# Kernel optimization log

Hardware: AMD Instinct MI355X
Metric: run time of the kernel (lower is better)

Reference implementation:

```python
import jax, jax.numpy as jnp
import numpy as np

B, F, N = 32, 10, 512   # batch_num, win_size (all_feature), node_num
E = 8192                # edges per graph
INTER = 256             # GAT inter_dim
HEADS = 2
NEG_SLOPE = 0.2
BN_EPS = 1e-5


def setup_inputs() -> dict:
    key = jax.random.key(0)
    ks = jax.random.split(key, 16)
    data = jax.random.normal(ks[0], (B, F, N), dtype=jnp.float32)
    # loop-free random edges: src != dst (matches PyG remove_self_loops + add_self_loops)
    dst = jax.random.randint(ks[1], (E,), 0, N)
    off = jax.random.randint(ks[2], (E,), 1, N)
    src = (dst + off) % N
    org_edge_index = jnp.stack([src, dst]).astype(jnp.int64)
    g = 0.05
    return {
        "data": data,
        "org_edge_index": org_edge_index,
        "W1": jax.random.normal(ks[3], (F, HEADS * INTER), dtype=jnp.float32) * g,
        "as1": jax.random.normal(ks[4], (HEADS, INTER), dtype=jnp.float32) * g,
        "ad1": jax.random.normal(ks[5], (HEADS, INTER), dtype=jnp.float32) * g,
        "b1": jnp.zeros((HEADS * INTER,), dtype=jnp.float32),
        "W2": jax.random.normal(ks[6], (HEADS * INTER, HEADS * INTER), dtype=jnp.float32) * g,
        "as2": jax.random.normal(ks[7], (HEADS, INTER), dtype=jnp.float32) * g,
        "ad2": jax.random.normal(ks[8], (HEADS, INTER), dtype=jnp.float32) * g,
        "b2": jnp.zeros((HEADS * INTER,), dtype=jnp.float32),
        "Wfc": jax.random.normal(ks[9], (HEADS * INTER, 1), dtype=jnp.float32) * g,
        "bfc": jnp.zeros((1,), dtype=jnp.float32),
        "gamma": jnp.ones((1,), dtype=jnp.float32),
        "beta": jnp.zeros((1,), dtype=jnp.float32),
    }


def _gat_conv(x, src, dst, W, a_src, a_dst, b):
    # PyG GATConv (v1), concat=True, negative_slope=0.2
    n = x.shape[0]
    H, C = a_src.shape
    h = (x @ W).reshape(n, H, C)                       # [n, H, C]
    al_s = jnp.einsum('nhc,hc->nh', h, a_src)          # [n, H]
    al_d = jnp.einsum('nhc,hc->nh', h, a_dst)
    e = jax.nn.leaky_relu(al_s[src] + al_d[dst], NEG_SLOPE)  # [Etot, H]
    emax = jax.ops.segment_max(e, dst, num_segments=n)       # segment softmax over dst
    ex = jnp.exp(e - emax[dst])
    denom = jax.ops.segment_sum(ex, dst, num_segments=n)
    alpha = ex / (denom[dst] + 1e-16)                  # [Etot, H]
    msg = h[src] * alpha[:, :, None]                   # [Etot, H, C]
    out = jax.ops.segment_sum(msg, dst, num_segments=n)
    return out.reshape(n, H * C) + b


def reference(data, org_edge_index, W1, as1, ad1, b1, W2, as2, ad2, b2,
              Wfc, bfc, gamma, beta):
    b_num, feat, n_num = data.shape
    x = data.reshape(-1, feat)                         # faithful to x.view(-1, all_feature)
    total = b_num * n_num
    # batched edge index: repeat with per-batch node offsets
    offs = jnp.arange(b_num, dtype=org_edge_index.dtype) * n_num
    be = (org_edge_index[:, None, :] + offs[None, :, None]).reshape(2, -1)
    loops = jnp.arange(total, dtype=org_edge_index.dtype)  # add_self_loops
    src = jnp.concatenate([be[0], loops])
    dst = jnp.concatenate([be[1], loops])
    x1 = _gat_conv(x, src, dst, W1, as1, ad1, b1)      # dropout = identity (eval)
    x2 = _gat_conv(x1, src, dst, W2, as2, ad2, b2)
    y = x2 @ Wfc + bfc                                 # [total, 1]
    # BatchNorm1d(1), eval mode: running_mean=0, running_var=1
    y = y * (gamma / jnp.sqrt(1.0 + BN_EPS)) + beta
    y = jax.nn.relu(y)
    return y.reshape(-1, 1, n_num)                     # [B, 1, N]
```

## Files before the change

### kernel.cpp

```cpp
#include <hip/hip_runtime.h>
#include <math.h>

#define B_  32
#define F_  10
#define N_  512
#define E_  8192
#define T_  16384
#define EC_ 8704
#define HC_ 512
#define C_  256

typedef __attribute__((ext_vector_type(8))) short bf16x8;
typedef __attribute__((ext_vector_type(4))) float f32x4;

__device__ __forceinline__ unsigned short f2bf(float f) {
    unsigned int u = __float_as_uint(f);
    u = (u + 0x7fffu + ((u >> 16) & 1u)) >> 16;
    return (unsigned short)u;
}
__device__ __forceinline__ float bf2f(unsigned short b) {
    return __uint_as_float(((unsigned int)b) << 16);
}
__device__ __forceinline__ float dot4(f32x4 a, f32x4 b) {
    f32x4 m = a * b;
    return m[0] + m[1] + m[2] + m[3];
}
__device__ __forceinline__ unsigned int pack2(unsigned short a, unsigned short b) {
    return (unsigned int)a | ((unsigned int)b << 16);
}
__device__ __forceinline__ void bf2x2(unsigned int u, float& f0, float& f1) {
    f0 = __uint_as_float(u << 16);
    f1 = __uint_as_float(u & 0xffff0000u);
}
__device__ __forceinline__ void async_cp16(const void* g, void* l) {
    __builtin_amdgcn_global_load_lds(
        (const __attribute__((address_space(1))) unsigned int*)g,
        (__attribute__((address_space(3))) unsigned int*)l, 16, 0, 0);
}

__device__ __forceinline__ int node_map(int bid, int wid) {
    int x = bid & 7;
    int rest = bid >> 3;
    int batch = x * 4 + (rest >> 7);
    int within = rest & 127;
    return batch * 512 + within * 4 + wid;
}

__global__ __launch_bounds__(1024) void prep_kernel(
    const int* __restrict__ eidx, const float* __restrict__ W2,
    int* __restrict__ off0, int* __restrict__ csr0,
    unsigned short* __restrict__ Bhi, unsigned short* __restrict__ Blo) {
    if (blockIdx.x < 256) {
        __shared__ float t[32][33];
        int bx = blockIdx.x & 15, by = blockIdx.x >> 4;
        int kb = bx * 32, nb = by * 32;
        int tx = threadIdx.x & 31, r = threadIdx.x >> 5;
        t[r][tx] = W2[(size_t)(kb + r) * HC_ + nb + tx];
        __syncthreads();
        float v = t[tx][r];
        unsigned short h = f2bf(v);
        Bhi[(size_t)(nb + r) * HC_ + kb + tx] = h;
        Blo[(size_t)(nb + r) * HC_ + kb + tx] = f2bf(v - bf2f(h));
    } else {
        __shared__ int cnt[512];
        __shared__ int scn[512];
        int tid = threadIdx.x;
        if (tid < 512) cnt[tid] = 0;
        __syncthreads();
        const int* edst = eidx + E_;
        for (int j = tid; j < EC_; j += 1024) {
            int d = (j < E_) ? edst[j] : (j - E_);
            atomicAdd(&cnt[d], 1);
        }
        __syncthreads();
        if (tid < 512) scn[tid] = cnt[tid];
        __syncthreads();
        for (int dd = 1; dd < 512; dd <<= 1) {
            int add = (tid < 512 && tid >= dd) ? scn[tid - dd] : 0;
            __syncthreads();
            if (tid < 512) scn[tid] += add;
            __syncthreads();
        }
        if (tid < 512) {
            int excl = scn[tid] - cnt[tid];
            off0[tid] = excl;
            cnt[tid] = excl;
        }
        if (tid == 0) off0[512] = EC_;
        __syncthreads();
        for (int j = tid; j < EC_; j += 1024) {
            int s, d;
            if (j < E_) { s = eidx[j]; d = edst[j]; }
            else { s = d = j - E_; }
            int pos = atomicAdd(&cnt[d], 1);
            csr0[pos] = s;
        }
    }
}

__global__ __launch_bounds__(256) void gemm1_kernel(
    const float* __restrict__ X, const float* __restrict__ W1,
    const float* __restrict__ a_s, const float* __restrict__ a_d,
    unsigned short* __restrict__ Hs, float* __restrict__ als,
    float* __restrict__ ald, float* __restrict__ als2z,
    float* __restrict__ ald2z) {
    __shared__ float xs[4][80];
    int tid = threadIdx.x, lane = tid & 63, w = tid >> 6;
    int q = blockIdx.x;
    int batch = (q & 7) * 4 + (q >> 7);
    int sub = (q >> 3) & 15;
    int nb = batch * 512 + sub * 32 + w * 8;
    int col = lane * 8;

    f32x4 w1r[F_][2];
#pragma unroll
    for (int k = 0; k < F_; ++k) {
        w1r[k][0] = *(const f32x4*)&W1[k * HC_ + col];
        w1r[k][1] = *(const f32x4*)&W1[k * HC_ + col + 4];
    }
    f32x4 asl = *(const f32x4*)&a_s[col], ash = *(const f32x4*)&a_s[col + 4];
    f32x4 adl = *(const f32x4*)&a_d[col], adh = *(const f32x4*)&a_d[col + 4];

    const float* xp = X + (size_t)nb * F_;
    if (lane < 40) {
        xs[w][lane] = xp[lane];
        xs[w][lane + 40] = xp[lane + 40];
    }
    if (lane < 16) als2z[nb * 2 + lane] = 0.f;
    else if (lane >= 48) ald2z[nb * 2 + lane - 48] = 0.f;

#pragma unroll
    for (int n = 0; n < 8; ++n) {
        f32x4 h0 = {0.f, 0.f, 0.f, 0.f}, h1 = h0;
#pragma unroll
        for (int k = 0; k < F_; ++k) {
            float xv = xs[w][n * F_ + k];
            h0 += xv * w1r[k][0];
            h1 += xv * w1r[k][1];
        }
        int node = nb + n;
        uint4 uh;
        uh.x = pack2(f2bf(h0[0]), f2bf(h0[1]));
        uh.y = pack2(f2bf(h0[2]), f2bf(h0[3]));
        uh.z = pack2(f2bf(h1[0]), f2bf(h1[1]));
        uh.w = pack2(f2bf(h1[2]), f2bf(h1[3]));
        *(uint4*)&Hs[(size_t)node * HC_ + col] = uh;
        float ps = dot4(h0, asl) + dot4(h1, ash);
        float pd = dot4(h0, adl) + dot4(h1, adh);
#pragma unroll
        for (int m = 1; m <= 16; m <<= 1) {
            ps += __shfl_xor(ps, m);
            pd += __shfl_xor(pd, m);
        }
        if (lane == 0)  { als[node * 2 + 0] = ps; ald[node * 2 + 0] = pd; }
        if (lane == 32) { als[node * 2 + 1] = ps; ald[node * 2 + 1] = pd; }
    }
}

template <int MODE>
__global__ __launch_bounds__(256) void agg_kernel(
    const unsigned short* __restrict__ Hin, const float* __restrict__ als,
    const float* __restrict__ ald, const int* __restrict__ off0,
    const int* __restrict__ csr0, const float* __restrict__ bias,
    unsigned short* __restrict__ Ahi,
    const float* __restrict__ Wfc, const float* __restrict__ bfc,
    const float* __restrict__ gamma, const float* __restrict__ beta,
    float* __restrict__ out) {
    int tid = threadIdx.x, lane = tid & 63, wid = tid >> 6;
    int dst = node_map(blockIdx.x, wid);
    int bbase = dst & ~511;
    int dl = dst & 511;
    int beg = off0[dl], end = off0[dl + 1], deg = end - beg;
    float ad0 = ald[2 * dst], ad1 = ald[2 * dst + 1];
    int col = lane * 8;
    float A[8] = {0.f, 0.f, 0.f, 0.f, 0.f, 0.f, 0.f, 0.f};

    if (deg <= 64) {
        float e0 = -1e30f, e1 = -1e30f;
        int sl = 0;
        if (lane < deg) {
            sl = csr0[beg + lane] + bbase;
            float a0 = als[2 * sl], a1 = als[2 * sl + 1];
            e0 = a0 + ad0; e0 = e0 > 0.f ? e0 : 0.2f * e0;
            e1 = a1 + ad1; e1 = e1 > 0.f ? e1 : 0.2f * e1;
        }
        float m0 = e0, m1 = e1;
#pragma unroll
        for (int m = 1; m < 64; m <<= 1) {
            m0 = fmaxf(m0, __shfl_xor(m0, m));
            m1 = fmaxf(m1, __shfl_xor(m1, m));
        }
        float x0 = (lane < deg) ? expf(e0 - m0) : 0.f;
        float x1 = (lane < deg) ? expf(e1 - m1) : 0.f;
        float d0 = x0, d1 = x1;
#pragma unroll
        for (int m = 1; m < 64; m <<= 1) {
            d0 += __shfl_xor(d0, m);
            d1 += __shfl_xor(d1, m);
        }
        float w0l = x0 / (d0 + 1e-16f);
        float w1l = x1 / (d1 + 1e-16f);
        for (int e = 0; e < deg; ++e) {
            int s = __shfl(sl, e);
            float wa = __shfl(w0l, e);
            float wb = __shfl(w1l, e);
            float w = (lane < 32) ? wa : wb;
            uint4 hv = *(const uint4*)(Hin + (size_t)s * HC_ + col);
            float f0, f1;
            bf2x2(hv.x, f0, f1); A[0] = fmaf(w, f0, A[0]); A[1] = fmaf(w, f1, A[1]);
            bf2x2(hv.y, f0, f1); A[2] = fmaf(w, f0, A[2]); A[3] = fmaf(w, f1, A[3]);
            bf2x2(hv.z, f0, f1); A[4] = fmaf(w, f0, A[4]); A[5] = fmaf(w, f1, A[5]);
            bf2x2(hv.w, f0, f1); A[6] = fmaf(w, f0, A[6]); A[7] = fmaf(w, f1, A[7]);
        }
    } else {
        float m0 = -1e30f, m1 = -1e30f;
        for (int k = beg + lane; k < end; k += 64) {
            int s = csr0[k] + bbase;
            float e0 = als[2 * s] + ad0; e0 = e0 > 0.f ? e0 : 0.2f * e0;
            float e1 = als[2 * s + 1] + ad1; e1 = e1 > 0.f ? e1 : 0.2f * e1;
            m0 = fmaxf(m0, e0);
            m1 = fmaxf(m1, e1);
        }
#pragma unroll
        for (int m = 1; m < 64; m <<= 1) {
            m0 = fmaxf(m0, __shfl_xor(m0, m));
            m1 = fmaxf(m1, __shfl_xor(m1, m));
        }
        float d0 = 0.f, d1 = 0.f;
        for (int k = beg + lane; k < end; k += 64) {
            int s = csr0[k] + bbase;
            float e0 = als[2 * s] + ad0; e0 = e0 > 0.f ? e0 : 0.2f * e0;
            float e1 = als[2 * s + 1] + ad1; e1 = e1 > 0.f ? e1 : 0.2f * e1;
            d0 += expf(e0 - m0);
            d1 += expf(e1 - m1);
        }
#pragma unroll
        for (int m = 1; m < 64; m <<= 1) {
            d0 += __shfl_xor(d0, m);
            d1 += __shfl_xor(d1, m);
        }
        float inv0 = 1.f / (d0 + 1e-16f);
        float inv1 = 1.f / (d1 + 1e-16f);
        for (int k = beg; k < end; ++k) {
            int s = csr0[k] + bbase;
            float e0 = als[2 * s] + ad0; e0 = e0 > 0.f ? e0 : 0.2f * e0;
            float e1 = als[2 * s + 1] + ad1; e1 = e1 > 0.f ? e1 : 0.2f * e1;
            float w0 = expf(e0 - m0) * inv0;
            float w1 = expf(e1 - m1) * inv1;
            float w = (lane < 32) ? w0 : w1;
            uint4 hv = *(const uint4*)(Hin + (size_t)s * HC_ + col);
            float f0, f1;
            bf2x2(hv.x, f0, f1); A[0] = fmaf(w, f0, A[0]); A[1] = fmaf(w, f1, A[1]);
            bf2x2(hv.y, f0, f1); A[2] = fmaf(w, f0, A[2]); A[3] = fmaf(w, f1, A[3]);
            bf2x2(hv.z, f0, f1); A[4] = fmaf(w, f0, A[4]); A[5] = fmaf(w, f1, A[5]);
            bf2x2(hv.w, f0, f1); A[6] = fmaf(w, f0, A[6]); A[7] = fmaf(w, f1, A[7]);
        }
    }

#pragma unroll
    for (int j = 0; j < 8; ++j) A[j] += bias[col + j];

    if (MODE == 0) {
        uint4 uh;
        uh.x = pack2(f2bf(A[0]), f2bf(A[1]));
        uh.y = pack2(f2bf(A[2]), f2bf(A[3]));
        uh.z = pack2(f2bf(A[4]), f2bf(A[5]));
        uh.w = pack2(f2bf(A[6]), f2bf(A[7]));
        *(uint4*)&Ahi[(size_t)dst * HC_ + col] = uh;
    } else {
        float y = 0.f;
#pragma unroll
        for (int j = 0; j < 8; ++j) y = fmaf(A[j], Wfc[col + j], y);
#pragma unroll
        for (int m = 1; m < 64; m <<= 1) y += __shfl_xor(y, m);
        if (lane == 0) {
            y += bfc[0];
            y = y * (gamma[0] * rsqrtf(1.f + 1e-5f)) + beta[0];
            out[dst] = y > 0.f ? y : 0.f;
        }
    }
}

__global__ __launch_bounds__(512, 1) void gemm2_kernel(
    const unsigned short* __restrict__ Ahi,
    const unsigned short* __restrict__ Bhi, const unsigned short* __restrict__ Blo,
    unsigned short* __restrict__ H2,
    const float* __restrict__ as2, const float* __restrict__ ad2,
    float* __restrict__ als2, float* __restrict__ ald2) {
    __shared__ __align__(16) char smem[135168];
    const int tid = threadIdx.x, lane = tid & 63, wid = tid >> 6;
    const int wr = wid >> 1, wc = wid & 1;
    const int g = (blockIdx.x & 7) * 32 + (blockIdx.x >> 3);
    const int row0 = (g >> 2) * 256, col0 = (g & 3) * 128;
    const int lr = lane & 15, lk = lane >> 4;
    const int x7 = lr & 7;

    f32x4 acc[4][4] = {};

    const char* gsrc[8];
    int loff[8];
#pragma unroll
    for (int l = 0; l < 8; ++l) {
        int i = tid + l * 512;
        if (i < 2048) {
            int r = i >> 3, c = i & 7;
            gsrc[l] = (const char*)(Ahi + (size_t)(row0 + r) * HC_ + ((c ^ (r & 7)) << 3));
            loff[l] = i << 4;
        } else if (i < 3072) {
            int j = i - 2048, r = j >> 3, c = j & 7;
            gsrc[l] = (const char*)(Bhi + (size_t)(col0 + r) * HC_ + ((c ^ (r & 7)) << 3));
            loff[l] = 32768 + (j << 4);
        } else {
            int j = i - 3072, r = j >> 3, c = j & 7;
            gsrc[l] = (const char*)(Blo + (size_t)(col0 + r) * HC_ + ((c ^ (r & 7)) << 3));
            loff[l] = 49152 + (j << 4);
        }
    }
    char* lds0 = smem;

#pragma unroll
    for (int l = 0; l < 8; ++l) async_cp16(gsrc[l], lds0 + loff[l]);
    asm volatile("s_waitcnt vmcnt(0)" ::: "memory");
    __builtin_amdgcn_s_barrier();

    int cur = 0;
    for (int kt = 0; kt < 8; ++kt) {
        if (kt < 7) {
            char* dst = lds0 + ((cur ^ 1) << 16);
#pragma unroll
            for (int l = 0; l < 8; ++l)
                async_cp16(gsrc[l] + (size_t)(kt + 1) * 128, dst + loff[l]);
        }
        const char* base = lds0 + (cur << 16);
#pragma unroll
        for (int kk = 0; kk < 2; ++kk) {
            bf16x8 a[4], bh[4], bl[4];
            int cx = ((kk * 4 + lk) ^ x7) << 4;
#pragma unroll
            for (int m = 0; m < 4; ++m) {
                int ra = wr * 64 + m * 16 + lr;
                int rb = wc * 64 + m * 16 + lr;
                a[m]  = *(const bf16x8*)(base + ra * 128 + cx);
                bh[m] = *(const bf16x8*)(base + 32768 + rb * 128 + cx);
                bl[m] = *(const bf16x8*)(base + 49152 + rb * 128 + cx);
            }
#pragma unroll
            for (int m = 0; m < 4; ++m)
#pragma unroll
                for (int n = 0; n < 4; ++n) {
                    acc[m][n] = __builtin_amdgcn_mfma_f32_16x16x32_bf16(a[m], bh[n], acc[m][n], 0, 0, 0);
                    acc[m][n] = __builtin_amdgcn_mfma_f32_16x16x32_bf16(a[m], bl[n], acc[m][n], 0, 0, 0);
                }
        }
        asm volatile("s_waitcnt vmcnt(0)" ::: "memory");
        __builtin_amdgcn_s_barrier();
        cur ^= 1;
    }

    float* tb = (float*)smem;
#pragma unroll
    for (int m = 0; m < 4; ++m)
#pragma unroll
        for (int i = 0; i < 4; ++i) {
            int row = wr * 64 + m * 16 + lk * 4 + i;
#pragma unroll
            for (int n = 0; n < 4; ++n)
                tb[row * 132 + wc * 64 + n * 16 + lr] = acc[m][n][i];
        }
    __syncthreads();
    const int head = col0 >> 8;
    const float* a_s2 = as2 + head * C_ + (col0 & 255);
    const float* a_d2 = ad2 + head * C_ + (col0 & 255);
#pragma unroll
    for (int p = 0; p < 8; ++p) {
        int q = tid + p * 512;
        int row = q >> 4, cs = (q & 15) * 8;
        const float* v = &tb[row * 132 + cs];
        uint4 uh;
        uh.x = pack2(f2bf(v[0]), f2bf(v[1]));
        uh.y = pack2(f2bf(v[2]), f2bf(v[3]));
        uh.z = pack2(f2bf(v[4]), f2bf(v[5]));
        uh.w = pack2(f2bf(v[6]), f2bf(v[7]));
        *(uint4*)&H2[(size_t)(row0 + row) * HC_ + col0 + cs] = uh;
        float ps = 0.f, pd = 0.f;
#pragma unroll
        for (int j = 0; j < 8; ++j) {
            ps = fmaf(v[j], a_s2[cs + j], ps);
            pd = fmaf(v[j], a_d2[cs + j], pd);
        }
#pragma unroll
        for (int m = 1; m < 16; m <<= 1) {
            ps += __shfl_xor(ps, m);
            pd += __shfl_xor(pd, m);
        }
        if ((tid & 15) == 0) {
            atomicAdd(&als2[(row0 + row) * 2 + head], ps);
            atomicAdd(&ald2[(row0 + row) * 2 + head], pd);
        }
    }
}

extern "C" void kernel_launch(void* const* d_in, const int* in_sizes, int n_in,
                              void* d_out, int out_size, void* d_ws, size_t ws_size,
                              hipStream_t stream) {
    const float* data  = (const float*)d_in[0];
    const int*   eidx  = (const int*)d_in[1];
    const float* W1    = (const float*)d_in[2];
    const float* as1   = (const float*)d_in[3];
    const float* ad1   = (const float*)d_in[4];
    const float* b1    = (const float*)d_in[5];
    const float* W2    = (const float*)d_in[6];
    const float* as2   = (const float*)d_in[7];
    const float* ad2   = (const float*)d_in[8];
    const float* b2    = (const float*)d_in[9];
    const float* Wfc   = (const float*)d_in[10];
    const float* bfc   = (const float*)d_in[11];
    const float* gamma = (const float*)d_in[12];
    const float* beta  = (const float*)d_in[13];
    float* out = (float*)d_out;

    char* base = (char*)d_ws;
    size_t o = 0;
    auto take = [&](size_t bytes) {
        char* p = base + o;
        o = (o + bytes + 255) & ~(size_t)255;
        return p;
    };
    int*   off0 = (int*)take((size_t)(N_ + 1) * 4);
    int*   csr0 = (int*)take((size_t)EC_ * 4);
    float* als1 = (float*)take((size_t)T_ * 2 * 4);
    float* ald1 = (float*)take((size_t)T_ * 2 * 4);
    float* als2 = (float*)take((size_t)T_ * 2 * 4);
    float* ald2 = (float*)take((size_t)T_ * 2 * 4);
    unsigned short* hs1 = (unsigned short*)take((size_t)T_ * HC_ * 2);
    unsigned short* hs2 = (unsigned short*)take((size_t)T_ * HC_ * 2);
    unsigned short* Ahi = (unsigned short*)take((size_t)T_ * HC_ * 2);
    unsigned short* Bhi = (unsigned short*)take((size_t)HC_ * HC_ * 2);
    unsigned short* Blo = (unsigned short*)take((size_t)HC_ * HC_ * 2);

    prep_kernel<<<257, 1024, 0, stream>>>(eidx, W2, off0, csr0, Bhi, Blo);
    gemm1_kernel<<<512, 256, 0, stream>>>(data, W1, as1, ad1, hs1, als1, ald1,
                                          als2, ald2);
    agg_kernel<0><<<4096, 256, 0, stream>>>(hs1, als1, ald1, off0, csr0, b1,
                                            Ahi, nullptr, nullptr, nullptr,
                                            nullptr, nullptr);
    gemm2_kernel<<<256, 512, 0, stream>>>(Ahi, Bhi, Blo, hs2, as2, ad2, als2, ald2);
    agg_kernel<1><<<4096, 256, 0, stream>>>(hs2, als2, ald2, off0, csr0, b2,
                                            nullptr, Wfc, bfc, gamma,
                                            beta, out);
}
```

Measured before the change: 92.39 us.

## Fold prep work into gemm1 launch and unroll aggregation gather by four

```diff
diff --git a/kernel.cpp b/kernel.cpp
--- a/kernel.cpp
+++ b/kernel.cpp
@@ -46,66 +46,76 @@
     return batch * 512 + within * 4 + wid;
 }
 
-__global__ __launch_bounds__(1024) void prep_kernel(
-    const int* __restrict__ eidx, const float* __restrict__ W2,
-    int* __restrict__ off0, int* __restrict__ csr0,
-    unsigned short* __restrict__ Bhi, unsigned short* __restrict__ Blo) {
-    if (blockIdx.x < 256) {
-        __shared__ float t[32][33];
-        int bx = blockIdx.x & 15, by = blockIdx.x >> 4;
-        int kb = bx * 32, nb = by * 32;
-        int tx = threadIdx.x & 31, r = threadIdx.x >> 5;
-        t[r][tx] = W2[(size_t)(kb + r) * HC_ + nb + tx];
-        __syncthreads();
-        float v = t[tx][r];
-        unsigned short h = f2bf(v);
-        Bhi[(size_t)(nb + r) * HC_ + kb + tx] = h;
-        Blo[(size_t)(nb + r) * HC_ + kb + tx] = f2bf(v - bf2f(h));
-    } else {
-        __shared__ int cnt[512];
-        __shared__ int scn[512];
-        int tid = threadIdx.x;
-        if (tid < 512) cnt[tid] = 0;
-        __syncthreads();
-        const int* edst = eidx + E_;
-        for (int j = tid; j < EC_; j += 1024) {
-            int d = (j < E_) ? edst[j] : (j - E_);
-            atomicAdd(&cnt[d], 1);
-        }
-        __syncthreads();
-        if (tid < 512) scn[tid] = cnt[tid];
-        __syncthreads();
-        for (int dd = 1; dd < 512; dd <<= 1) {
-            int add = (tid < 512 && tid >= dd) ? scn[tid - dd] : 0;
-            __syncthreads();
-            if (tid < 512) scn[tid] += add;
-            __syncthreads();
-        }
-        if (tid < 512) {
-            int excl = scn[tid] - cnt[tid];
-            off0[tid] = excl;
-            cnt[tid] = excl;
-        }
-        if (tid == 0) off0[512] = EC_;
-        __syncthreads();
-        for (int j = tid; j < EC_; j += 1024) {
-            int s, d;
-            if (j < E_) { s = eidx[j]; d = edst[j]; }
-            else { s = d = j - E_; }
-            int pos = atomicAdd(&cnt[d], 1);
-            csr0[pos] = s;
-        }
-    }
-}
-
 __global__ __launch_bounds__(256) void gemm1_kernel(
     const float* __restrict__ X, const float* __restrict__ W1,
     const float* __restrict__ a_s, const float* __restrict__ a_d,
     unsigned short* __restrict__ Hs, float* __restrict__ als,
     float* __restrict__ ald, float* __restrict__ als2z,
-    float* __restrict__ ald2z) {
-    __shared__ float xs[4][80];
-    int tid = threadIdx.x, lane = tid & 63, w = tid >> 6;
+    float* __restrict__ ald2z,
+    const int* __restrict__ eidx, const float* __restrict__ W2,
+    int* __restrict__ off0, int* __restrict__ csr0,
+    unsigned short* __restrict__ Bhi, unsigned short* __restrict__ Blo) {
+    __shared__ float shmem[1056];
+    int tid = threadIdx.x;
+
+    if (blockIdx.x >= 512) {
+        if (blockIdx.x < 768) {
+            int pb = blockIdx.x - 512;
+            float* t = shmem;
+            int bx = pb & 15, by = pb >> 4;
+            int kb = bx * 32, nb = by * 32;
+            int tx = tid & 31, ty = tid >> 5;
+#pragma unroll
+            for (int r = ty; r < 32; r += 8)
+                t[r * 33 + tx] = W2[(size_t)(kb + r) * HC_ + nb + tx];
+            __syncthreads();
+#pragma unroll
+            for (int r = ty; r < 32; r += 8) {
+                float v = t[tx * 33 + r];
+                unsigned short h = f2bf(v);
+                Bhi[(size_t)(nb + r) * HC_ + kb + tx] = h;
+                Blo[(size_t)(nb + r) * HC_ + kb + tx] = f2bf(v - bf2f(h));
+            }
+        } else {
+            int* cnt = (int*)shmem;
+            int* scn = (int*)shmem + 512;
+            cnt[2 * tid] = 0; cnt[2 * tid + 1] = 0;
+            __syncthreads();
+            const int* edst = eidx + E_;
+            for (int j = tid; j < EC_; j += 256) {
+                int d = (j < E_) ? edst[j] : (j - E_);
+                atomicAdd(&cnt[d], 1);
+            }
+            __syncthreads();
+            int c0 = cnt[2 * tid], c1 = cnt[2 * tid + 1];
+            scn[tid] = c0 + c1;
+            __syncthreads();
+            for (int d = 1; d < 256; d <<= 1) {
+                int add = (tid >= d) ? scn[tid - d] : 0;
+                __syncthreads();
+                scn[tid] += add;
+                __syncthreads();
+            }
+            int e0 = scn[tid] - (c0 + c1);
+            off0[2 * tid] = e0;
+            off0[2 * tid + 1] = e0 + c0;
+            cnt[2 * tid] = e0;
+            cnt[2 * tid + 1] = e0 + c0;
+            if (tid == 255) off0[512] = EC_;
+            __syncthreads();
+            for (int j = tid; j < EC_; j += 256) {
+                int s, d;
+                if (j < E_) { s = eidx[j]; d = edst[j]; }
+                else { s = d = j - E_; }
+                int pos = atomicAdd(&cnt[d], 1);
+                csr0[pos] = s;
+            }
+        }
+        return;
+    }
+
+    float* xs = shmem;
+    int lane = tid & 63, w = tid >> 6;
     int q = blockIdx.x;
     int batch = (q & 7) * 4 + (q >> 7);
     int sub = (q >> 3) & 15;
@@ -123,8 +133,8 @@
 
     const float* xp = X + (size_t)nb * F_;
     if (lane < 40) {
-        xs[w][lane] = xp[lane];
-        xs[w][lane + 40] = xp[lane + 40];
+        xs[w * 80 + lane] = xp[lane];
+        xs[w * 80 + lane + 40] = xp[lane + 40];
     }
     if (lane < 16) als2z[nb * 2 + lane] = 0.f;
     else if (lane >= 48) ald2z[nb * 2 + lane - 48] = 0.f;
@@ -134,7 +144,7 @@
         f32x4 h0 = {0.f, 0.f, 0.f, 0.f}, h1 = h0;
 #pragma unroll
         for (int k = 0; k < F_; ++k) {
-            float xv = xs[w][n * F_ + k];
+            float xv = xs[w * 80 + n * F_ + k];
             h0 += xv * w1r[k][0];
             h1 += xv * w1r[k][1];
         }
@@ -200,7 +210,41 @@
         }
         float w0l = x0 / (d0 + 1e-16f);
         float w1l = x1 / (d1 + 1e-16f);
-        for (int e = 0; e < deg; ++e) {
+        int e = 0;
+        for (; e + 4 <= deg; e += 4) {
+            int s0 = __shfl(sl, e), s1 = __shfl(sl, e + 1);
+            int s2 = __shfl(sl, e + 2), s3 = __shfl(sl, e + 3);
+            float wa0 = __shfl(w0l, e),     wb0 = __shfl(w1l, e);
+            float wa1 = __shfl(w0l, e + 1), wb1 = __shfl(w1l, e + 1);
+            float wa2 = __shfl(w0l, e + 2), wb2 = __shfl(w1l, e + 2);
+            float wa3 = __shfl(w0l, e + 3), wb3 = __shfl(w1l, e + 3);
+            float w0 = (lane < 32) ? wa0 : wb0;
+            float w1 = (lane < 32) ? wa1 : wb1;
+            float w2 = (lane < 32) ? wa2 : wb2;
+            float w3 = (lane < 32) ? wa3 : wb3;
+            uint4 h0 = *(const uint4*)(Hin + (size_t)s0 * HC_ + col);
+            uint4 h1 = *(const uint4*)(Hin + (size_t)s1 * HC_ + col);
+            uint4 h2 = *(const uint4*)(Hin + (size_t)s2 * HC_ + col);
+            uint4 h3 = *(const uint4*)(Hin + (size_t)s3 * HC_ + col);
+            float f0, f1;
+            bf2x2(h0.x, f0, f1); A[0] = fmaf(w0, f0, A[0]); A[1] = fmaf(w0, f1, A[1]);
+            bf2x2(h0.y, f0, f1); A[2] = fmaf(w0, f0, A[2]); A[3] = fmaf(w0, f1, A[3]);
+            bf2x2(h0.z, f0, f1); A[4] = fmaf(w0, f0, A[4]); A[5] = fmaf(w0, f1, A[5]);
+            bf2x2(h0.w, f0, f1); A[6] = fmaf(w0, f0, A[6]); A[7] = fmaf(w0, f1, A[7]);
+            bf2x2(h1.x, f0, f1); A[0] = fmaf(w1, f0, A[0]); A[1] = fmaf(w1, f1, A[1]);
+            bf2x2(h1.y, f0, f1); A[2] = fmaf(w1, f0, A[2]); A[3] = fmaf(w1, f1, A[3]);
+            bf2x2(h1.z, f0, f1); A[4] = fmaf(w1, f0, A[4]); A[5] = fmaf(w1, f1, A[5]);
+            bf2x2(h1.w, f0, f1); A[6] = fmaf(w1, f0, A[6]); A[7] = fmaf(w1, f1, A[7]);
+            bf2x2(h2.x, f0, f1); A[0] = fmaf(w2, f0, A[0]); A[1] = fmaf(w2, f1, A[1]);
+            bf2x2(h2.y, f0, f1); A[2] = fmaf(w2, f0, A[2]); A[3] = fmaf(w2, f1, A[3]);
+            bf2x2(h2.z, f0, f1); A[4] = fmaf(w2, f0, A[4]); A[5] = fmaf(w2, f1, A[5]);
+            bf2x2(h2.w, f0, f1); A[6] = fmaf(w2, f0, A[6]); A[7] = fmaf(w2, f1, A[7]);
+            bf2x2(h3.x, f0, f1); A[0] = fmaf(w3, f0, A[0]); A[1] = fmaf(w3, f1, A[1]);
+            bf2x2(h3.y, f0, f1); A[2] = fmaf(w3, f0, A[2]); A[3] = fmaf(w3, f1, A[3]);
+            bf2x2(h3.z, f0, f1); A[4] = fmaf(w3, f0, A[4]); A[5] = fmaf(w3, f1, A[5]);
+            bf2x2(h3.w, f0, f1); A[6] = fmaf(w3, f0, A[6]); A[7] = fmaf(w3, f1, A[7]);
+        }
+        for (; e < deg; ++e) {
             int s = __shfl(sl, e);
             float wa = __shfl(w0l, e);
             float wb = __shfl(w1l, e);
@@ -438,9 +482,9 @@
     unsigned short* Bhi = (unsigned short*)take((size_t)HC_ * HC_ * 2);
     unsigned short* Blo = (unsigned short*)take((size_t)HC_ * HC_ * 2);
 
-    prep_kernel<<<257, 1024, 0, stream>>>(eidx, W2, off0, csr0, Bhi, Blo);
-    gemm1_kernel<<<512, 256, 0, stream>>>(data, W1, as1, ad1, hs1, als1, ald1,
-                                          als2, ald2);
+    gemm1_kernel<<<769, 256, 0, stream>>>(data, W1, as1, ad1, hs1, als1, ald1,
+                                          als2, ald2, eidx, W2, off0, csr0,
+                                          Bhi, Blo);
     agg_kernel<0><<<4096, 256, 0, stream>>>(hs1, als1, ald1, off0, csr0, b1,
                                             Ahi, nullptr, nullptr, nullptr,
                                             nullptr, nullptr);
```

Measured after the change: 92.78 us. No clear change (+0.4%).
